# Optimization experiments

Hardware: AMD Instinct MI355X
Metric: run time of the kernel (lower is better)

Reference implementation:

```python
import jax, jax.numpy as jnp
import numpy as np

B, N, D = 8, 2048, 512

def setup_inputs() -> dict:
    key = jax.random.key(0)
    k1, k2, k3, k4 = jax.random.split(key, 4)
    x = jax.random.normal(k1, (B, N, D), dtype=jnp.float32)
    x2 = jax.random.normal(k2, (B, N, D), dtype=jnp.float32)
    # nn.Linear(dim, dim): weight [D, D], bias [D]
    W = jax.random.normal(k3, (D, D), dtype=jnp.float32) * (1.0 / np.sqrt(D))
    b = jax.random.normal(k4, (D,), dtype=jnp.float32) * 0.01
    return {"x": x, "x2": x2, "W": W, "b": b}

def reference(x, x2, W, b):
    # key = softmax(x2.transpose(1,2), dim=1) -> softmax over feature axis D,
    # shape [B, D, N]; equivalently softmax(x2, axis=-1) then transpose.
    key_t = jax.nn.softmax(x2, axis=-1)          # [B, N, D], softmax over D
    query = jax.nn.softmax(x2, axis=1)            # [B, N, D], softmax over N
    # context = value @ key : [B,N,D] @ [B,D,N] -> [B,N,N]
    context = jnp.einsum('bnd,bmd->bnm', x, key_t)
    # atten = context @ query : [B,N,N] @ [B,N,D] -> [B,N,D]
    atten = jnp.einsum('bnm,bmd->bnd', context, query)
    # linear projection: atten @ W.T + b
    return jnp.einsum('bnd,ed->bne', atten, W) + b
```

## Files before the change

kernel.cpp:

```cpp
#include <hip/hip_runtime.h>


typedef __attribute__((ext_vector_type(8))) short          s16x8;
typedef __attribute__((ext_vector_type(8))) unsigned short u16x8;
typedef __attribute__((ext_vector_type(4))) float          f32x4;

#define B_ 8
#define N_ 2048
#define D_ 512

__device__ inline unsigned short f2bf(float f) {
    unsigned u = __float_as_uint(f);
    u += 0x7FFFu + ((u >> 16) & 1u);
    return (unsigned short)(u >> 16);
}

__global__ __launch_bounds__(256) void rowsum_exp_k(const float* __restrict__ x2,
                                                    float* __restrict__ rks) {
    int w = threadIdx.x >> 6, l = threadIdx.x & 63;
    int r = blockIdx.x * 4 + w;
    const float* p = x2 + (size_t)r * D_ + l * 8;
    float4 a = *(const float4*)p;
    float4 b = *(const float4*)(p + 4);
    float s = __expf(a.x) + __expf(a.y) + __expf(a.z) + __expf(a.w)
            + __expf(b.x) + __expf(b.y) + __expf(b.z) + __expf(b.w);
#pragma unroll
    for (int off = 1; off < 64; off <<= 1) s += __shfl_xor(s, off);
    if (l == 0) rks[r] = 1.0f / s;
}

__global__ __launch_bounds__(512) void colsum_exp_k(const float* __restrict__ x2,
                                                    float* __restrict__ qs) {
    int d = threadIdx.x;
    int b = blockIdx.y, mc = blockIdx.x;
    const float* p = x2 + ((size_t)b * N_ + (size_t)mc * 128) * D_ + d;
    float s = 0.f;
#pragma unroll 4
    for (int mm = 0; mm < 128; ++mm) s += __expf(p[(size_t)mm * D_]);
    atomicAdd(&qs[b * D_ + d], s);
}

__global__ __launch_bounds__(256) void softmax_tr_k(const float* __restrict__ x2,
                                                    const float* __restrict__ rks,
                                                    const float* __restrict__ qs,
                                                    unsigned short* __restrict__ Kt,
                                                    unsigned short* __restrict__ Qt) {
    __shared__ unsigned short kt[64][65], qt[64][65];
    int b = blockIdx.z, d0 = blockIdx.y * 64, m0 = blockIdx.x * 64;
    int tx = threadIdx.x & 63, w = threadIdx.x >> 6;
    float rq = 1.0f / qs[b * D_ + d0 + tx];
#pragma unroll
    for (int it = 0; it < 16; ++it) {
        int row = w * 16 + it;
        float v = x2[((size_t)b * N_ + m0 + row) * D_ + d0 + tx];
        float e = __expf(v);
        float rk = rks[b * N_ + m0 + row];
        kt[tx][row] = f2bf(e * rk);
        qt[tx][row] = f2bf(e * rq);
    }
    __syncthreads();
#pragma unroll
    for (int it = 0; it < 16; ++it) {
        int dr = w * 16 + it;
        size_t off = ((size_t)b * D_ + d0 + dr) * N_ + m0 + tx;
        Kt[off] = kt[dr][tx];
        Qt[off] = qt[dr][tx];
    }
}

__global__ __launch_bounds__(256) void cvt_bf16_k(const float* __restrict__ in,
                                                  unsigned short* __restrict__ out) {
    size_t i = ((size_t)blockIdx.x * 256 + threadIdx.x) * 8;
    float4 a = *(const float4*)(in + i);
    float4 b = *(const float4*)(in + i + 4);
    u16x8 o;
    o[0] = f2bf(a.x); o[1] = f2bf(a.y); o[2] = f2bf(a.z); o[3] = f2bf(a.w);
    o[4] = f2bf(b.x); o[5] = f2bf(b.y); o[6] = f2bf(b.z); o[7] = f2bf(b.w);
    *(u16x8*)(out + i) = o;
}

__device__ inline void gload16(const unsigned short* g, unsigned short* l) {
    __builtin_amdgcn_global_load_lds((const __attribute__((address_space(1))) void*)g,
                                     (__attribute__((address_space(3))) void*)l, 16, 0, 0);
}

template <bool OUT_BF16, bool BIAS>
__global__ __launch_bounds__(256, 2) void gemm_bt_k(const unsigned short* __restrict__ A,
                                                    const unsigned short* __restrict__ Bm,
                                                    void* __restrict__ Cv,
                                                    const float* __restrict__ bias,
                                                    int M, int N, int K,
                                                    long long sA, long long sB, long long sC) {
    __shared__ unsigned short As[128 * 32], Bs[128 * 32];
    int b = blockIdx.z;
    const unsigned short* Ab = A + (size_t)b * sA;
    const unsigned short* Bb = Bm + (size_t)b * sB;
    int tm = blockIdx.y, tn = blockIdx.x;
    int tid = threadIdx.x, w = tid >> 6, l = tid & 63;
    int wr = w >> 1, wc = w & 1;
    int lr = l & 15, lg = l >> 4;

    f32x4 acc[4][4];
#pragma unroll
    for (int i = 0; i < 4; ++i)
#pragma unroll
        for (int j = 0; j < 4; ++j) acc[i][j] = (f32x4){0.f, 0.f, 0.f, 0.f};

    const int rowbase = tm * 128, colbase = tn * 128;

    for (int kt = 0; kt < K; kt += 32) {
#pragma unroll
        for (int i = 0; i < 2; ++i) {
            int ci = (i * 4 + w) * 64 + l;
            int row = ci >> 2, cc = ci & 3;
            gload16(Ab + (size_t)(rowbase + row) * K + kt + cc * 8, As + (i * 4 + w) * 512);
            gload16(Bb + (size_t)(colbase + row) * K + kt + cc * 8, Bs + (i * 4 + w) * 512);
        }
        __syncthreads();
        s16x8 af[4], bf[4];
#pragma unroll
        for (int i = 0; i < 4; ++i)
            af[i] = *(const s16x8*)&As[(wr * 64 + i * 16 + lr) * 32 + lg * 8];
#pragma unroll
        for (int j = 0; j < 4; ++j)
            bf[j] = *(const s16x8*)&Bs[(wc * 64 + j * 16 + lr) * 32 + lg * 8];
#pragma unroll
        for (int i = 0; i < 4; ++i)
#pragma unroll
            for (int j = 0; j < 4; ++j)
                acc[i][j] = __builtin_amdgcn_mfma_f32_16x16x32_bf16(af[i], bf[j], acc[i][j], 0, 0, 0);
        __syncthreads();
    }

    if (OUT_BF16) {
        unsigned short* C = (unsigned short*)Cv + (size_t)b * sC;
#pragma unroll
        for (int i = 0; i < 4; ++i)
#pragma unroll
            for (int j = 0; j < 4; ++j) {
                int col = colbase + wc * 64 + j * 16 + lr;
#pragma unroll
                for (int r = 0; r < 4; ++r) {
                    int row = rowbase + wr * 64 + i * 16 + lg * 4 + r;
                    C[(size_t)row * N + col] = f2bf(acc[i][j][r]);
                }
            }
    } else {
        float* C = (float*)Cv + (size_t)b * sC;
#pragma unroll
        for (int i = 0; i < 4; ++i)
#pragma unroll
            for (int j = 0; j < 4; ++j) {
                int col = colbase + wc * 64 + j * 16 + lr;
                float bv = BIAS ? bias[col] : 0.f;
#pragma unroll
                for (int r = 0; r < 4; ++r) {
                    int row = rowbase + wr * 64 + i * 16 + lg * 4 + r;
                    C[(size_t)row * N + col] = acc[i][j][r] + bv;
                }
            }
    }
}

extern "C" void kernel_launch(void* const* d_in, const int* in_sizes, int n_in,
                              void* d_out, int out_size, void* d_ws, size_t ws_size,
                              hipStream_t stream) {
    const float* x    = (const float*)d_in[0];
    const float* x2   = (const float*)d_in[1];
    const float* W    = (const float*)d_in[2];
    const float* bias = (const float*)d_in[3];
    float* out = (float*)d_out;

    unsigned short* Kt = (unsigned short*)d_ws;
    unsigned short* Qt = Kt + 8388608;
    unsigned short* xb = Qt + 8388608;
    unsigned short* Wb = xb + 8388608;
    unsigned short* KQ = Wb + 262144;
    unsigned short* Mt = KQ + 2097152;
    float* rks = (float*)(Mt + 2097152);
    float* qs  = rks + 16384;

    hipMemsetAsync(qs, 0, (size_t)B_ * D_ * sizeof(float), stream);

    rowsum_exp_k<<<dim3(B_ * N_ / 4), 256, 0, stream>>>(x2, rks);
    colsum_exp_k<<<dim3(16, B_), 512, 0, stream>>>(x2, qs);

    softmax_tr_k<<<dim3(N_ / 64, D_ / 64, B_), 256, 0, stream>>>(x2, rks, qs, Kt, Qt);

    cvt_bf16_k<<<dim3(4096), 256, 0, stream>>>(x, xb);
    cvt_bf16_k<<<dim3(128), 256, 0, stream>>>(W, Wb);

    gemm_bt_k<true, false><<<dim3(4, 4, B_), 256, 0, stream>>>(
        Kt, Qt, KQ, nullptr, 512, 512, 2048,
        (long long)512 * 2048, (long long)512 * 2048, (long long)512 * 512);

    gemm_bt_k<true, false><<<dim3(4, 4, B_), 256, 0, stream>>>(
        Wb, KQ, Mt, nullptr, 512, 512, 512,
        0LL, (long long)512 * 512, (long long)512 * 512);

    gemm_bt_k<false, true><<<dim3(4, 16, B_), 256, 0, stream>>>(
        xb, Mt, out, bias, 2048, 512, 512,
        (long long)2048 * 512, (long long)512 * 512, (long long)2048 * 512);
}
```

Baseline: 208.0 us.

## Fuse row/col exp sums and split-K smaller-tile GEMMs for more parallelism

Merges the row-sum and column-sum passes over x2 into one kernel. Each block computes per-row softmax denominators and accumulates column partials in shared memory, then issues atomics. The K^T·Q GEMM (K=2048) moves to a 64x64-tile kernel with split-K=2 and fp32 atomic accumulation, followed by a bf16 conversion pass. The W·KQ GEMM also uses 64x64 tiles. Previously these GEMMs launched only 128 blocks; the goal is better occupancy of the CUs. The cost is a larger memset, atomic traffic, and an extra conversion kernel.

```diff
diff --git a/kernel.cpp b/kernel.cpp
--- a/kernel.cpp
+++ b/kernel.cpp
@@ -15,29 +15,37 @@
     return (unsigned short)(u >> 16);
 }
 
-__global__ __launch_bounds__(256) void rowsum_exp_k(const float* __restrict__ x2,
-                                                    float* __restrict__ rks) {
+__global__ __launch_bounds__(256) void fused_sums_k(const float* __restrict__ x2,
+                                                    float* __restrict__ rks,
+                                                    float* __restrict__ qs) {
+    __shared__ float cp[4][512];
     int w = threadIdx.x >> 6, l = threadIdx.x & 63;
-    int r = blockIdx.x * 4 + w;
-    const float* p = x2 + (size_t)r * D_ + l * 8;
-    float4 a = *(const float4*)p;
-    float4 b = *(const float4*)(p + 4);
-    float s = __expf(a.x) + __expf(a.y) + __expf(a.z) + __expf(a.w)
-            + __expf(b.x) + __expf(b.y) + __expf(b.z) + __expf(b.w);
-#pragma unroll
-    for (int off = 1; off < 64; off <<= 1) s += __shfl_xor(s, off);
-    if (l == 0) rks[r] = 1.0f / s;
-}
-
-__global__ __launch_bounds__(512) void colsum_exp_k(const float* __restrict__ x2,
-                                                    float* __restrict__ qs) {
-    int d = threadIdx.x;
-    int b = blockIdx.y, mc = blockIdx.x;
-    const float* p = x2 + ((size_t)b * N_ + (size_t)mc * 128) * D_ + d;
-    float s = 0.f;
-#pragma unroll 4
-    for (int mm = 0; mm < 128; ++mm) s += __expf(p[(size_t)mm * D_]);
-    atomicAdd(&qs[b * D_ + d], s);
+    int rbase = blockIdx.x * 32;
+    int b = rbase / N_;
+    const int c0 = l * 8;
+    float colacc[8] = {0.f, 0.f, 0.f, 0.f, 0.f, 0.f, 0.f, 0.f};
+#pragma unroll
+    for (int rr = 0; rr < 8; ++rr) {
+        int r = rbase + w * 8 + rr;
+        const float* p = x2 + (size_t)r * D_ + c0;
+        float4 a = *(const float4*)p;
+        float4 bb = *(const float4*)(p + 4);
+        float e0 = __expf(a.x), e1 = __expf(a.y), e2 = __expf(a.z), e3 = __expf(a.w);
+        float e4 = __expf(bb.x), e5 = __expf(bb.y), e6 = __expf(bb.z), e7 = __expf(bb.w);
+        float s = e0 + e1 + e2 + e3 + e4 + e5 + e6 + e7;
+#pragma unroll
+        for (int off = 1; off < 64; off <<= 1) s += __shfl_xor(s, off);
+        if (l == 0) rks[r] = 1.0f / s;
+        colacc[0] += e0; colacc[1] += e1; colacc[2] += e2; colacc[3] += e3;
+        colacc[4] += e4; colacc[5] += e5; colacc[6] += e6; colacc[7] += e7;
+    }
+#pragma unroll
+    for (int c = 0; c < 8; ++c) cp[w][c0 + c] = colacc[c];
+    __syncthreads();
+    for (int c = threadIdx.x; c < 512; c += 256) {
+        float s = cp[0][c] + cp[1][c] + cp[2][c] + cp[3][c];
+        atomicAdd(&qs[b * D_ + c], s);
+    }
 }
 
 __global__ __launch_bounds__(256) void softmax_tr_k(const float* __restrict__ x2,
@@ -84,10 +92,81 @@
                                      (__attribute__((address_space(3))) void*)l, 16, 0, 0);
 }
 
-template <bool OUT_BF16, bool BIAS>
+template <int MODE>
+__global__ __launch_bounds__(256, 4) void gemm64_k(const unsigned short* __restrict__ A,
+                                                   const unsigned short* __restrict__ Bm,
+                                                   void* __restrict__ Cv,
+                                                   int M, int N, int K, int nsplit,
+                                                   long long sA, long long sB, long long sC) {
+    __shared__ unsigned short As[64 * 32], Bs[64 * 32];
+    int b = blockIdx.z / nsplit, ks = blockIdx.z % nsplit;
+    int klen = K / nsplit, k0 = ks * klen;
+    const unsigned short* Ab = A + (size_t)b * sA;
+    const unsigned short* Bb = Bm + (size_t)b * sB;
+    int tid = threadIdx.x, w = tid >> 6, l = tid & 63;
+    int wr = w >> 1, wc = w & 1;
+    int lr = l & 15, lg = l >> 4;
+    int srow = tid >> 2, scc = tid & 3;
+
+    f32x4 acc[2][2];
+#pragma unroll
+    for (int i = 0; i < 2; ++i)
+#pragma unroll
+        for (int j = 0; j < 2; ++j) acc[i][j] = (f32x4){0.f, 0.f, 0.f, 0.f};
+
+    const int rowbase = blockIdx.y * 64, colbase = blockIdx.x * 64;
+
+    for (int kt = k0; kt < k0 + klen; kt += 32) {
+        gload16(Ab + (size_t)(rowbase + srow) * K + kt + scc * 8, As + w * 512);
+        gload16(Bb + (size_t)(colbase + srow) * K + kt + scc * 8, Bs + w * 512);
+        __syncthreads();
+        s16x8 af[2], bf[2];
+#pragma unroll
+        for (int i = 0; i < 2; ++i)
+            af[i] = *(const s16x8*)&As[(wr * 32 + i * 16 + lr) * 32 + lg * 8];
+#pragma unroll
+        for (int j = 0; j < 2; ++j)
+            bf[j] = *(const s16x8*)&Bs[(wc * 32 + j * 16 + lr) * 32 + lg * 8];
+#pragma unroll
+        for (int i = 0; i < 2; ++i)
+#pragma unroll
+            for (int j = 0; j < 2; ++j)
+                acc[i][j] = __builtin_amdgcn_mfma_f32_16x16x32_bf16(af[i], bf[j], acc[i][j], 0, 0, 0);
+        __syncthreads();
+    }
+
+    if (MODE == 0) {
+        float* C = (float*)Cv + (size_t)b * sC;
+#pragma unroll
+        for (int i = 0; i < 2; ++i)
+#pragma unroll
+            for (int j = 0; j < 2; ++j) {
+                int col = colbase + wc * 32 + j * 16 + lr;
+#pragma unroll
+                for (int r = 0; r < 4; ++r) {
+                    int row = rowbase + wr * 32 + i * 16 + lg * 4 + r;
+                    atomicAdd(&C[(size_t)row * N + col], acc[i][j][r]);
+                }
+            }
+    } else {
+        unsigned short* C = (unsigned short*)Cv + (size_t)b * sC;
+#pragma unroll
+        for (int i = 0; i < 2; ++i)
+#pragma unroll
+            for (int j = 0; j < 2; ++j) {
+                int col = colbase + wc * 32 + j * 16 + lr;
+#pragma unroll
+                for (int r = 0; r < 4; ++r) {
+                    int row = rowbase + wr * 32 + i * 16 + lg * 4 + r;
+                    C[(size_t)row * N + col] = f2bf(acc[i][j][r]);
+                }
+            }
+    }
+}
+
 __global__ __launch_bounds__(256, 2) void gemm_bt_k(const unsigned short* __restrict__ A,
                                                     const unsigned short* __restrict__ Bm,
-                                                    void* __restrict__ Cv,
+                                                    float* __restrict__ Cv,
                                                     const float* __restrict__ bias,
                                                     int M, int N, int K,
                                                     long long sA, long long sB, long long sC) {
@@ -132,34 +211,19 @@
         __syncthreads();
     }
 
-    if (OUT_BF16) {
-        unsigned short* C = (unsigned short*)Cv + (size_t)b * sC;
-#pragma unroll
-        for (int i = 0; i < 4; ++i)
-#pragma unroll
-            for (int j = 0; j < 4; ++j) {
-                int col = colbase + wc * 64 + j * 16 + lr;
-#pragma unroll
-                for (int r = 0; r < 4; ++r) {
-                    int row = rowbase + wr * 64 + i * 16 + lg * 4 + r;
-                    C[(size_t)row * N + col] = f2bf(acc[i][j][r]);
-                }
+    float* C = Cv + (size_t)b * sC;
+#pragma unroll
+    for (int i = 0; i < 4; ++i)
+#pragma unroll
+        for (int j = 0; j < 4; ++j) {
+            int col = colbase + wc * 64 + j * 16 + lr;
+            float bv = bias[col];
+#pragma unroll
+            for (int r = 0; r < 4; ++r) {
+                int row = rowbase + wr * 64 + i * 16 + lg * 4 + r;
+                C[(size_t)row * N + col] = acc[i][j][r] + bv;
             }
-    } else {
-        float* C = (float*)Cv + (size_t)b * sC;
-#pragma unroll
-        for (int i = 0; i < 4; ++i)
-#pragma unroll
-            for (int j = 0; j < 4; ++j) {
-                int col = colbase + wc * 64 + j * 16 + lr;
-                float bv = BIAS ? bias[col] : 0.f;
-#pragma unroll
-                for (int r = 0; r < 4; ++r) {
-                    int row = rowbase + wr * 64 + i * 16 + lg * 4 + r;
-                    C[(size_t)row * N + col] = acc[i][j][r] + bv;
-                }
-            }
-    }
+        }
 }
 
 extern "C" void kernel_launch(void* const* d_in, const int* in_sizes, int n_in,
@@ -171,34 +235,36 @@
     const float* bias = (const float*)d_in[3];
     float* out = (float*)d_out;
 
-    unsigned short* Kt = (unsigned short*)d_ws;
-    unsigned short* Qt = Kt + 8388608;
-    unsigned short* xb = Qt + 8388608;
-    unsigned short* Wb = xb + 8388608;
-    unsigned short* KQ = Wb + 262144;
-    unsigned short* Mt = KQ + 2097152;
-    float* rks = (float*)(Mt + 2097152);
-    float* qs  = rks + 16384;
-
-    hipMemsetAsync(qs, 0, (size_t)B_ * D_ * sizeof(float), stream);
-
-    rowsum_exp_k<<<dim3(B_ * N_ / 4), 256, 0, stream>>>(x2, rks);
-    colsum_exp_k<<<dim3(16, B_), 512, 0, stream>>>(x2, qs);
+    unsigned short* Kt  = (unsigned short*)d_ws;
+    unsigned short* Qt  = Kt + 8388608;
+    unsigned short* xb  = Qt + 8388608;
+    unsigned short* Wb  = xb + 8388608;
+    unsigned short* KQb = Wb + 262144;
+    unsigned short* Mt  = KQb + 2097152;
+    float* KQf = (float*)(Mt + 2097152);
+    float* qs  = KQf + 2097152;
+    float* rks = qs + 4096;
+
+    hipMemsetAsync(KQf, 0, (2097152 + 4096) * sizeof(float), stream);
+
+    fused_sums_k<<<dim3(B_ * N_ / 32), 256, 0, stream>>>(x2, rks, qs);
 
     softmax_tr_k<<<dim3(N_ / 64, D_ / 64, B_), 256, 0, stream>>>(x2, rks, qs, Kt, Qt);
 
     cvt_bf16_k<<<dim3(4096), 256, 0, stream>>>(x, xb);
     cvt_bf16_k<<<dim3(128), 256, 0, stream>>>(W, Wb);
 
-    gemm_bt_k<true, false><<<dim3(4, 4, B_), 256, 0, stream>>>(
-        Kt, Qt, KQ, nullptr, 512, 512, 2048,
+    gemm64_k<0><<<dim3(8, 8, B_ * 2), 256, 0, stream>>>(
+        Kt, Qt, KQf, 512, 512, 2048, 2,
         (long long)512 * 2048, (long long)512 * 2048, (long long)512 * 512);
 
-    gemm_bt_k<true, false><<<dim3(4, 4, B_), 256, 0, stream>>>(
-        Wb, KQ, Mt, nullptr, 512, 512, 512,
+    cvt_bf16_k<<<dim3(1024), 256, 0, stream>>>(KQf, KQb);
+
+    gemm64_k<2><<<dim3(8, 8, B_), 256, 0, stream>>>(
+        Wb, KQb, Mt, 512, 512, 512, 1,
         0LL, (long long)512 * 512, (long long)512 * 512);
 
-    gemm_bt_k<false, true><<<dim3(4, 16, B_), 256, 0, stream>>>(
+    gemm_bt_k<<<dim3(4, 16, B_), 256, 0, stream>>>(
         xb, Mt, out, bias, 2048, 512, 512,
         (long long)2048 * 512, (long long)512 * 512, (long long)2048 * 512);
 }
```

Measured after the change: 193.5 us. 1.08x faster.
